# Kernel tuning notes

Hardware: AMD Instinct MI355X
Metric: run time of the kernel (lower is better)

The kernel has to match this reference:

```python
import jax, jax.numpy as jnp
import numpy as np

N_NODES = 100000
N_EDGES = 1_600_000
F_IN = 128
N_HEADS = 4
F_OUT = 32


def setup_inputs() -> dict:
    key = jax.random.key(0)
    k1, k2, k3, k4, k5 = jax.random.split(key, 5)
    h_in = jax.random.normal(k1, (N_NODES, F_IN), dtype=jnp.float32)
    edge_index = jax.random.randint(k2, (2, N_EDGES), 0, N_NODES, dtype=jnp.int64)
    # Xavier-uniform-ish scales
    W = jax.random.normal(k3, (F_IN, N_HEADS * F_OUT), dtype=jnp.float32) * (1.0 / np.sqrt(F_IN))
    b = jnp.zeros((N_HEADS * F_OUT,), dtype=jnp.float32)
    a_src = jax.random.normal(k4, (N_HEADS, F_OUT), dtype=jnp.float32) * 0.1
    a_tgt = jax.random.normal(k5, (N_HEADS, F_OUT), dtype=jnp.float32) * 0.1
    return {"h_in": h_in, "edge_index": edge_index, "W": W, "b": b, "a_src": a_src, "a_tgt": a_tgt}


def reference(h_in, edge_index, W, b, a_src, a_tgt):
    # Eval mode: dropout is identity.
    src, tgt = edge_index[0], edge_index[1]
    # Shared linear projection: [N, H, F]
    h_proj = (h_in @ W + b).reshape(-1, N_HEADS, F_OUT)
    # Per-node attention score contributions: [N, H]
    score_src = jnp.einsum('nhf,hf->nh', h_proj, a_src)
    score_tgt = jnp.einsum('nhf,hf->nh', h_proj, a_tgt)
    # Edge-level scores (gather), LeakyReLU(0.2) as in the original: [E, H]
    e = jax.nn.leaky_relu(score_tgt[tgt] + score_src[src], negative_slope=0.2)
    # Segment softmax over incoming edges of each target node.
    # (Original uses raw exp without max subtraction; replicate faithfully.)
    exp_e = jnp.exp(e)
    denom = jax.ops.segment_sum(exp_e, tgt, num_segments=N_NODES)  # [N, H]
    alpha = exp_e / (denom[tgt] + 1e-16)                            # [E, H]
    # Weighted message aggregation: [N, H, F]
    msg = alpha[:, :, None] * h_proj[src]                           # [E, H, F]
    h_new = jax.ops.segment_sum(msg, tgt, num_segments=N_NODES)
    # concat=True branch: original computes activation(new_features) but returns
    # the UN-activated concatenated view (new_features_sigm is unused) -> replicate.
    return h_new.reshape(N_NODES, N_HEADS * F_OUT)
```

## Files before the change

kernel.cpp:

```cpp
#include <hip/hip_runtime.h>
#include <hip/hip_bf16.h>

typedef unsigned short u16;
typedef unsigned int u32;
typedef long long i64;
typedef __attribute__((ext_vector_type(8))) short s8v;
typedef __attribute__((ext_vector_type(4))) float f32x4;

#define SUBCAP 1023
#define BKT_CAP (8 * SUBCAP)

__device__ __forceinline__ float bf2f(u16 u) {
    union { u32 i; float f; } x; x.i = ((u32)u) << 16; return x.f;
}
__device__ __forceinline__ u16 f2bf(float f) {
    union { float f; u32 i; } x; x.f = f;
    u32 v = x.i;
    u32 r = v + 0x7FFFu + ((v >> 16) & 1u);
    return (u16)(r >> 16);
}
__device__ __forceinline__ int get_i(const void* p, size_t i, int m64) {
    return m64 ? (int)((const i64*)p)[i] : ((const int*)p)[i];
}
__device__ __forceinline__ float lrelu_clamp(float v) {
    v = v > 0.f ? v : 0.2f * v;
    return fminf(v, 80.f);
}

__global__ __launch_bounds__(256) void k_init(
    const u16* __restrict__ hin, const int* __restrict__ eidx, int* __restrict__ flags,
    const u16* __restrict__ W, const float* __restrict__ Wf,
    const float* __restrict__ biasf, const float* __restrict__ asrcf,
    const float* __restrict__ atgtf,
    u16* __restrict__ Wt, u16* __restrict__ Wt_hi, u16* __restrict__ Wt_lo,
    float* __restrict__ wa, float* __restrict__ ba,
    int* __restrict__ bucket_cnt, int ncnt)
{
    const int b = blockIdx.x, t = threadIdx.x;
    if (b == 0) {
        __shared__ int c1, c2;
        if (t == 0) { c1 = 0; c2 = 0; }
        __syncthreads();
        int l1 = 0, l2 = 0;
        for (int i = t; i < 8192; i += 256) {
            float v = bf2f(hin[i]);
            if (!(fabsf(v) <= 100.f)) l1++;
            if ((i & 1) && eidx[i] == 0) l2++;
        }
        atomicAdd(&c1, l1); atomicAdd(&c2, l2);
        __syncthreads();
        if (t == 0) {
            flags[0] = (c1 > 40) ? 1 : 0;
            flags[1] = (c2 > 3000) ? 1 : 0;
        }
    } else if (b <= 64) {
        int i = (b - 1) * 256 + t;
        int k = i >> 7, n = i & 127;
        Wt[(size_t)n * 128 + k] = W[(size_t)k * 128 + n];
        float wf = Wf[(size_t)k * 128 + n];
        u16 hi = f2bf(wf);
        Wt_hi[(size_t)n * 128 + k] = hi;
        Wt_lo[(size_t)n * 128 + k] = f2bf(wf - bf2f(hi));
    } else if (b <= 68) {
        int idx = (b - 65) * 256 + t;
        int sel = idx >> 9, rem = idx & 511;
        int h = rem >> 7, k = rem & 127;
        const float* av = sel ? atgtf : asrcf;
        float s = 0.f;
        #pragma unroll 8
        for (int f = 0; f < 32; f++)
            s += Wf[(size_t)k * 128 + h * 32 + f] * av[h * 32 + f];
        wa[idx] = s;
    } else {
        if (t < 8) {
            int sel = t >> 2, h = t & 3;
            const float* av = sel ? atgtf : asrcf;
            float s = 0.f;
            #pragma unroll 8
            for (int f = 0; f < 32; f++)
                s += biasf[h * 32 + f] * av[h * 32 + f];
            ba[t] = s;
        }
    }
    for (int i = b * 256 + t; i < ncnt; i += gridDim.x * 256) bucket_cnt[i] = 0;
}

__global__ __launch_bounds__(256) void k_bktA(
    const void* __restrict__ eidx, const int* __restrict__ flags,
    int* __restrict__ bucket_cnt, u32* __restrict__ bkt,
    int n_edges, int n_nodes, int nbk)
{
    __shared__ int2 ed[4096];
    __shared__ int lcnt[512];
    __shared__ int lpos[512];
    const int t = threadIdx.x;
    const int e0 = blockIdx.x * 4096;
    const int rep = blockIdx.x & 7;
    const int m64 = flags[1];
    const int nloc = min(4096, n_edges - e0);

    for (int i = t; i < 512; i += 256) lcnt[i] = 0;
    __syncthreads();

    for (int r = 0; r < 16; r++) {
        int i = r * 256 + t;
        if (i < nloc) {
            int e = e0 + i;
            int s  = get_i(eidx, e, m64);
            int tg = get_i(eidx, (size_t)n_edges + e, m64);
            s  = min(max(s, 0), n_nodes - 1);
            tg = min(max(tg, 0), n_nodes - 1);
            ed[i] = make_int2(s, tg);
            atomicAdd(&lcnt[tg >> 8], 1);
        }
    }
    __syncthreads();

    for (int bb = t; bb < nbk; bb += 256) {
        int c = lcnt[bb];
        lpos[bb] = c ? atomicAdd(&bucket_cnt[rep * 512 + bb], c) : 0;
    }
    __syncthreads();

    for (int r = 0; r < 16; r++) {
        int i = r * 256 + t;
        if (i < nloc) {
            int2 st = ed[i];
            int bb = st.y >> 8;
            int p = atomicAdd(&lpos[bb], 1);
            p = min(p, SUBCAP - 1);
            bkt[(size_t)bb * BKT_CAP + rep * SUBCAP + p] =
                ((u32)st.x << 8) | (u32)(st.y & 255);
        }
    }
}

__global__ __launch_bounds__(256) void k_bsort(
    const int* __restrict__ bucket_cnt, const u32* __restrict__ bkt,
    int* __restrict__ offs, int* __restrict__ src_sorted,
    int n_edges, int n_nodes, int nbk)
{
    __shared__ int s_a[512], s_b[512];
    __shared__ int tcnt[256], tpos[256];
    __shared__ int subcnt[8];
    __shared__ int Gb_sh, total_sh;
    const int t = threadIdx.x;
    const int b = blockIdx.x;

    for (int i = t; i < 512; i += 256) {
        int tot = 0;
        if (i < nbk) {
            #pragma unroll
            for (int r = 0; r < 8; r++) tot += min(bucket_cnt[r * 512 + i], SUBCAP);
        }
        s_a[i] = tot;
    }
    if (t < 8) subcnt[t] = min(bucket_cnt[t * 512 + b], SUBCAP);
    __syncthreads();

    int* pa = s_a; int* pb = s_b;
    for (int off = 1; off < 512; off <<= 1) {
        #pragma unroll
        for (int k = 0; k < 2; k++) {
            int i = t + k * 256;
            pb[i] = pa[i] + (i >= off ? pa[i - off] : 0);
        }
        __syncthreads();
        int* sw = pa; pa = pb; pb = sw;
    }
    if (t == 0) {
        int run = 0;
        #pragma unroll
        for (int r = 0; r < 8; r++) run += subcnt[r];
        Gb_sh = pa[b] - run;
        total_sh = pa[511];
    }
    __syncthreads();
    const int Gb = Gb_sh, total = total_sh;

    tcnt[t] = 0;
    __syncthreads();
    const u32* mybkt = bkt + (size_t)b * BKT_CAP;
    #pragma unroll
    for (int r = 0; r < 8; r++) {
        const int c = subcnt[r];
        const u32* sub = mybkt + r * SUBCAP;
        for (int i = t; i < c; i += 256)
            atomicAdd(&tcnt[sub[i] & 255], 1);
    }
    __syncthreads();

    int own = tcnt[t];
    s_a[t] = own;
    __syncthreads();
    for (int off = 1; off < 256; off <<= 1) {
        int x = (t >= off) ? s_a[t - off] : 0;
        __syncthreads();
        s_a[t] += x;
        __syncthreads();
    }
    const int texcl = s_a[t] - own;

    const int tgt_id = b * 256 + t;
    if (tgt_id < n_nodes) offs[tgt_id] = Gb + texcl;
    if (b == 0 && t == 0) offs[n_nodes] = total;
    tpos[t] = Gb + texcl;
    __syncthreads();
    #pragma unroll
    for (int r = 0; r < 8; r++) {
        const int c = subcnt[r];
        const u32* sub = mybkt + r * SUBCAP;
        for (int i = t; i < c; i += 256) {
            u32 v = sub[i];
            int p = atomicAdd(&tpos[v & 255], 1);
            src_sorted[p] = (int)(v >> 8);
        }
    }
}

__global__ __launch_bounds__(256) void k_proj_mfma(
    const u16* __restrict__ hin, const u16* __restrict__ Wt,
    const u16* __restrict__ bias, const u16* __restrict__ a_src,
    const u16* __restrict__ a_tgt, const int* __restrict__ flags,
    u16* __restrict__ hp, float* __restrict__ ssrc, float* __restrict__ stgt,
    int M)
{
    if (flags[0]) return;
    const int lane = threadIdx.x & 63;
    const int q = lane >> 4, col = lane & 15;
    const int row0 = blockIdx.x * 64 + (threadIdx.x >> 6) * 16;
    if (row0 >= M) return;

    const int arow = min(row0 + col, M - 1);
    f32x4 acc[8];
    #pragma unroll
    for (int ct = 0; ct < 8; ct++) acc[ct] = (f32x4){0.f, 0.f, 0.f, 0.f};

    #pragma unroll
    for (int kc = 0; kc < 4; kc++) {
        s8v afrag = *(const s8v*)(hin + (size_t)arow * 128 + kc * 32 + q * 8);
        #pragma unroll
        for (int ct = 0; ct < 8; ct++) {
            s8v bfrag = *(const s8v*)(Wt + (size_t)(ct * 16 + col) * 128 + kc * 32 + q * 8);
            acc[ct] = __builtin_amdgcn_mfma_f32_16x16x32_bf16(afrag, bfrag, acc[ct], 0, 0, 0);
        }
    }

    float bb[8], as[8], at[8];
    #pragma unroll
    for (int ct = 0; ct < 8; ct++) {
        int c = ct * 16 + col;
        bb[ct] = bf2f(bias[c]);
        as[ct] = bf2f(a_src[c]);
        at[ct] = bf2f(a_tgt[c]);
    }

    #pragma unroll
    for (int r = 0; r < 4; r++) {
        int row = row0 + q * 4 + r;
        float ps0 = 0.f, ps1 = 0.f, ps2 = 0.f, ps3 = 0.f;
        float pt0 = 0.f, pt1 = 0.f, pt2 = 0.f, pt3 = 0.f;
        float ov[8];
        #pragma unroll
        for (int ct = 0; ct < 8; ct++) {
            float v = acc[ct][r] + bb[ct];
            ov[ct] = v;
            float s = v * as[ct], t2 = v * at[ct];
            if (ct < 2)      { ps0 += s; pt0 += t2; }
            else if (ct < 4) { ps1 += s; pt1 += t2; }
            else if (ct < 6) { ps2 += s; pt2 += t2; }
            else             { ps3 += s; pt3 += t2; }
        }
        if (row < M) {
            union { ushort4 h[2]; uint4 qv; } pk;
            pk.h[0] = make_ushort4(f2bf(ov[0]), f2bf(ov[1]), f2bf(ov[2]), f2bf(ov[3]));
            pk.h[1] = make_ushort4(f2bf(ov[4]), f2bf(ov[5]), f2bf(ov[6]), f2bf(ov[7]));
            *(uint4*)(hp + (size_t)row * 128 + col * 8) = pk.qv;
        }
        #pragma unroll
        for (int m = 1; m < 16; m <<= 1) {
            ps0 += __shfl_xor(ps0, m); ps1 += __shfl_xor(ps1, m);
            ps2 += __shfl_xor(ps2, m); ps3 += __shfl_xor(ps3, m);
            pt0 += __shfl_xor(pt0, m); pt1 += __shfl_xor(pt1, m);
            pt2 += __shfl_xor(pt2, m); pt3 += __shfl_xor(pt3, m);
        }
        if (row < M && col < 4) {
            float vs = col == 0 ? ps0 : col == 1 ? ps1 : col == 2 ? ps2 : ps3;
            float vt = col == 0 ? pt0 : col == 1 ? pt1 : col == 2 ? pt2 : pt3;
            ssrc[(size_t)row * 4 + col] = vs;
            stgt[(size_t)row * 4 + col] = vt;
        }
    }
}

__global__ __launch_bounds__(256) void k_proj_fm(
    const float* __restrict__ hin, const u16* __restrict__ Wt_hi,
    const u16* __restrict__ Wt_lo, const float* __restrict__ biasf,
    const float* __restrict__ wa, const float* __restrict__ ba,
    const int* __restrict__ flags,
    u16* __restrict__ hp, float* __restrict__ ssrc, float* __restrict__ stgt,
    int M)
{
    if (!flags[0]) return;
    __shared__ float wal[1032];
    const int t = threadIdx.x;
    for (int i = t; i < 1024; i += 256) wal[i] = wa[i];
    if (t < 8) wal[1024 + t] = ba[t];
    __syncthreads();

    const int lane = t & 63;
    const int q = lane >> 4, col = lane & 15;
    const int row0 = blockIdx.x * 64 + (t >> 6) * 16;
    if (row0 >= M) return;
    const int arow = min(row0 + col, M - 1);

    f32x4 acc[8];
    #pragma unroll
    for (int ct = 0; ct < 8; ct++) acc[ct] = (f32x4){0.f, 0.f, 0.f, 0.f};
    float ps[4] = {0.f, 0.f, 0.f, 0.f}, pt[4] = {0.f, 0.f, 0.f, 0.f};

    #pragma unroll
    for (int kc = 0; kc < 4; kc++) {
        const int ko = kc * 32 + q * 8;
        const float* hrow = hin + (size_t)arow * 128 + ko;
        float4 hva = *(const float4*)hrow;
        float4 hvb = *(const float4*)(hrow + 4);
        float hv[8] = {hva.x, hva.y, hva.z, hva.w, hvb.x, hvb.y, hvb.z, hvb.w};
        s8v ahi, alo;
        #pragma unroll
        for (int j = 0; j < 8; j++) {
            u16 hi = f2bf(hv[j]);
            ahi[j] = (short)hi;
            alo[j] = (short)f2bf(hv[j] - bf2f(hi));
        }
        #pragma unroll
        for (int ct = 0; ct < 8; ct++) {
            const size_t boff = (size_t)(ct * 16 + col) * 128 + ko;
            s8v bhi = *(const s8v*)(Wt_hi + boff);
            s8v blo = *(const s8v*)(Wt_lo + boff);
            acc[ct] = __builtin_amdgcn_mfma_f32_16x16x32_bf16(ahi, bhi, acc[ct], 0, 0, 0);
            acc[ct] = __builtin_amdgcn_mfma_f32_16x16x32_bf16(ahi, blo, acc[ct], 0, 0, 0);
            acc[ct] = __builtin_amdgcn_mfma_f32_16x16x32_bf16(alo, bhi, acc[ct], 0, 0, 0);
        }
        #pragma unroll
        for (int h = 0; h < 4; h++) {
            float4 sa = *(const float4*)&wal[h * 128 + ko];
            float4 sb = *(const float4*)&wal[h * 128 + ko + 4];
            ps[h] += hv[0] * sa.x + hv[1] * sa.y + hv[2] * sa.z + hv[3] * sa.w
                   + hv[4] * sb.x + hv[5] * sb.y + hv[6] * sb.z + hv[7] * sb.w;
            float4 ta = *(const float4*)&wal[512 + h * 128 + ko];
            float4 tb = *(const float4*)&wal[512 + h * 128 + ko + 4];
            pt[h] += hv[0] * ta.x + hv[1] * ta.y + hv[2] * ta.z + hv[3] * ta.w
                   + hv[4] * tb.x + hv[5] * tb.y + hv[6] * tb.z + hv[7] * tb.w;
        }
    }

    #pragma unroll
    for (int h = 0; h < 4; h++) {
        ps[h] += __shfl_xor(ps[h], 16); ps[h] += __shfl_xor(ps[h], 32);
        pt[h] += __shfl_xor(pt[h], 16); pt[h] += __shfl_xor(pt[h], 32);
    }
    if (q == 0 && row0 + col < M) {
        #pragma unroll
        for (int h = 0; h < 4; h++) {
            ssrc[(size_t)(row0 + col) * 4 + h] = ps[h] + wal[1024 + h];
            stgt[(size_t)(row0 + col) * 4 + h] = pt[h] + wal[1028 + h];
        }
    }

    float bb[8];
    #pragma unroll
    for (int ct = 0; ct < 8; ct++) bb[ct] = biasf[ct * 16 + col];
    #pragma unroll
    for (int r = 0; r < 4; r++) {
        int row = row0 + q * 4 + r;
        if (row < M) {
            union { ushort4 h[2]; uint4 qv; } pk;
            pk.h[0] = make_ushort4(f2bf(acc[0][r] + bb[0]), f2bf(acc[1][r] + bb[1]),
                                   f2bf(acc[2][r] + bb[2]), f2bf(acc[3][r] + bb[3]));
            pk.h[1] = make_ushort4(f2bf(acc[4][r] + bb[4]), f2bf(acc[5][r] + bb[5]),
                                   f2bf(acc[6][r] + bb[6]), f2bf(acc[7][r] + bb[7]));
            *(uint4*)(hp + (size_t)row * 128 + col * 8) = pk.qv;
        }
    }
}

__global__ __launch_bounds__(256) void k_agg_csr(
    const int* __restrict__ offs, const int* __restrict__ src_sorted,
    const float* __restrict__ ssrc, const float* __restrict__ stgt,
    const void* __restrict__ hp, void* __restrict__ out,
    const int* __restrict__ flags, int n_nodes)
{
    __shared__ u16 ob[4][128];
    __shared__ float obf[4][128];
    const int wave = threadIdx.x >> 6;
    int wid = (blockIdx.x * 256 + threadIdx.x) >> 6;
    wid = min(wid, n_nodes - 1);
    const int lane = threadIdx.x & 63;
    const int fp32 = flags[0];
    const int d0 = offs[wid], d1 = offs[wid + 1];

    const int sub = lane >> 4;
    const int li = lane & 15;
    const u16* hpb = (const u16*)hp;
    const float4* ssrc4 = (const float4*)ssrc;
    const float4 st4 = ((const float4*)stgt)[wid];
    const int deg = d1 - d0;

    float a[8] = {};
    auto accum = [&](float4 w, uint4 v) {
        a[0] += w.x * bf2f((u16)(v.x & 0xffff));
        a[1] += w.x * bf2f((u16)(v.x >> 16));
        a[2] += w.y * bf2f((u16)(v.y & 0xffff));
        a[3] += w.y * bf2f((u16)(v.y >> 16));
        a[4] += w.z * bf2f((u16)(v.z & 0xffff));
        a[5] += w.z * bf2f((u16)(v.z >> 16));
        a[6] += w.w * bf2f((u16)(v.w & 0xffff));
        a[7] += w.w * bf2f((u16)(v.w >> 16));
    };

    const int nh = min(deg, 64);
    int my_s = 0;
    float4 my_w = make_float4(0.f, 0.f, 0.f, 0.f);
    if (nh > 0) {
        my_s = src_sorted[d0 + min(lane, nh - 1)];
        float4 cs = ssrc4[my_s];
        if (lane < nh) {
            my_w = make_float4(__expf(lrelu_clamp(cs.x + st4.x)),
                               __expf(lrelu_clamp(cs.y + st4.y)),
                               __expf(lrelu_clamp(cs.z + st4.z)),
                               __expf(lrelu_clamp(cs.w + st4.w)));
        }
    }

    const int ns = (nh + 3) >> 2;
    auto sload = [&](int k, uint4& vv) {
        if (k < ns) {
            int s = __shfl(my_s, k * 4 + sub);
            vv = *(const uint4*)(hpb + (size_t)s * 128 + li * 8);
        }
    };
    auto sacc = [&](int k, uint4 vv) {
        if (k < ns) {
            int idx = k * 4 + sub;
            float4 w;
            w.x = __shfl(my_w.x, idx);
            w.y = __shfl(my_w.y, idx);
            w.z = __shfl(my_w.z, idx);
            w.w = __shfl(my_w.w, idx);
            accum(w, vv);
        }
    };
    uint4 v0{}, v1{}, v2{}, v3{}, v4{}, v5{}, v6{}, v7{};
    sload(0, v0); sload(1, v1); sload(2, v2); sload(3, v3);
    sload(4, v4); sload(5, v5); sload(6, v6); sload(7, v7);
    sacc(0, v0); sload(8, v0);
    sacc(1, v1); sload(9, v1);
    sacc(2, v2); sload(10, v2);
    sacc(3, v3); sload(11, v3);
    sacc(4, v4); sload(12, v4);
    sacc(5, v5); sload(13, v5);
    sacc(6, v6); sload(14, v6);
    sacc(7, v7); sload(15, v7);
    sacc(8, v0); sacc(9, v1); sacc(10, v2); sacc(11, v3);
    sacc(12, v4); sacc(13, v5); sacc(14, v6); sacc(15, v7);

    float4 es_t = make_float4(0.f, 0.f, 0.f, 0.f);
    if (deg > 64) {
        for (int e = d0 + 64; e < d1; e += 4) {
            int idx = e + sub;
            int ok = idx < d1;
            int s = src_sorted[ok ? idx : d1 - 1];
            uint4 v = *(const uint4*)(hpb + (size_t)s * 128 + li * 8);
            float4 cs = ssrc4[s];
            float4 w = make_float4(__expf(lrelu_clamp(cs.x + st4.x)),
                                   __expf(lrelu_clamp(cs.y + st4.y)),
                                   __expf(lrelu_clamp(cs.z + st4.z)),
                                   __expf(lrelu_clamp(cs.w + st4.w)));
            if (!ok) w = make_float4(0.f, 0.f, 0.f, 0.f);
            accum(w, v);
            es_t.x += w.x; es_t.y += w.y; es_t.z += w.z; es_t.w += w.w;
        }
    }

    float4 es = my_w;
    #pragma unroll
    for (int m = 1; m < 16; m <<= 1) {
        es.x += __shfl_xor(es.x, m);
        es.y += __shfl_xor(es.y, m);
        es.z += __shfl_xor(es.z, m);
        es.w += __shfl_xor(es.w, m);
    }
    es.x += es_t.x; es.y += es_t.y; es.z += es_t.z; es.w += es_t.w;

    #pragma unroll
    for (int m = 0; m < 8; m++) {
        a[m] += __shfl_xor(a[m], 16);
        a[m] += __shfl_xor(a[m], 32);
    }
    es.x += __shfl_xor(es.x, 16); es.x += __shfl_xor(es.x, 32);
    es.y += __shfl_xor(es.y, 16); es.y += __shfl_xor(es.y, 32);
    es.z += __shfl_xor(es.z, 16); es.z += __shfl_xor(es.z, 32);
    es.w += __shfl_xor(es.w, 16); es.w += __shfl_xor(es.w, 32);

    float inv4[4] = {1.f / (es.x + 1e-16f), 1.f / (es.y + 1e-16f),
                     1.f / (es.z + 1e-16f), 1.f / (es.w + 1e-16f)};

    if (!fp32) {
        if (sub == 0) {
            #pragma unroll
            for (int m = 0; m < 8; m++)
                ob[wave][m * 16 + li] = f2bf(a[m] * inv4[m >> 1]);
        }
        __syncthreads();
        if (sub == 0) {
            uint4 ov = *(const uint4*)&ob[wave][li * 8];
            *(uint4*)((u16*)out + (size_t)wid * 128 + li * 8) = ov;
        }
    } else {
        if (sub == 0) {
            #pragma unroll
            for (int m = 0; m < 8; m++)
                obf[wave][m * 16 + li] = a[m] * inv4[m >> 1];
        }
        __syncthreads();
        float* of = (float*)out + (size_t)wid * 128;
        *(float2*)(of + lane * 2) = make_float2(obf[wave][lane * 2],
                                                obf[wave][lane * 2 + 1]);
    }
}

extern "C" void kernel_launch(void* const* d_in, const int* in_sizes, int n_in,
                              void* d_out, int out_size, void* d_ws, size_t ws_size,
                              hipStream_t stream)
{
    const void* h_in  = d_in[0];
    const void* eidx  = d_in[1];
    const void* W     = d_in[2];
    const void* bias  = d_in[3];
    const void* a_src = d_in[4];
    const void* a_tgt = d_in[5];

    const int n_nodes = in_sizes[0] / 128;
    const int n_edges = in_sizes[1] / 2;
    const int nbk = (n_nodes + 255) >> 8;
    const int nba = (n_edges + 4095) / 4096;

    char* p = (char*)d_ws;
    auto alloc = [&](size_t bytes) { char* q = p; p += (bytes + 255) & ~(size_t)255; return q; };
    int*   flags      = (int*)  alloc(256);
    void*  hp         = (void*) alloc((size_t)n_nodes * 128 * sizeof(float));
    u16*   Wt         = (u16*)  alloc(128 * 128 * sizeof(u16));
    u16*   Wt_hi      = (u16*)  alloc(128 * 128 * sizeof(u16));
    u16*   Wt_lo      = (u16*)  alloc(128 * 128 * sizeof(u16));
    float* wa         = (float*)alloc(1024 * sizeof(float));
    float* ba         = (float*)alloc(8 * sizeof(float));
    float* ssrc       = (float*)alloc((size_t)n_nodes * 4 * sizeof(float));
    float* stgt       = (float*)alloc((size_t)n_nodes * 4 * sizeof(float));
    int*   offs       = (int*)  alloc(((size_t)n_nodes + 1) * sizeof(int));
    int*   bucket_cnt = (int*)  alloc(8 * 512 * sizeof(int));
    int*   src_sorted = (int*)  alloc((size_t)n_edges * sizeof(int));

    size_t bkt_bytes = (size_t)nbk * BKT_CAP * sizeof(u32);
    u32* bkt;
    if (bkt_bytes <= (size_t)n_nodes * 128 * 2)
        bkt = (u32*)((char*)hp + (size_t)n_nodes * 128 * 2);
    else
        bkt = (u32*)alloc(bkt_bytes);

    k_init     <<<70, 256, 0, stream>>>((const u16*)h_in, (const int*)eidx, flags,
                                        (const u16*)W, (const float*)W,
                                        (const float*)bias, (const float*)a_src,
                                        (const float*)a_tgt,
                                        Wt, Wt_hi, Wt_lo, wa, ba,
                                        bucket_cnt, 8 * 512);
    k_bktA     <<<nba, 256, 0, stream>>>(eidx, flags, bucket_cnt, bkt,
                                         n_edges, n_nodes, nbk);
    k_bsort    <<<nbk, 256, 0, stream>>>(bucket_cnt, bkt, offs, src_sorted,
                                         n_edges, n_nodes, nbk);
    k_proj_mfma<<<(n_nodes + 63) / 64, 256, 0, stream>>>((const u16*)h_in, Wt, (const u16*)bias,
                                                         (const u16*)a_src, (const u16*)a_tgt,
                                                         flags, (u16*)hp, ssrc, stgt, n_nodes);
    k_proj_fm  <<<(n_nodes + 63) / 64, 256, 0, stream>>>((const float*)h_in, Wt_hi, Wt_lo,
                                                         (const float*)bias, wa, ba,
                                                         flags, (u16*)hp, ssrc, stgt, n_nodes);
    k_agg_csr  <<<(n_nodes + 3) / 4, 256, 0, stream>>>(offs, src_sorted, ssrc, stgt,
                                                       hp, d_out, flags, n_nodes);
}
```

Baseline: 307.9 us.

## Quantize projected features to int8 with per-row scale and merge projection kernels

The projected node features are stored as int8 with a per-row absmax scale instead of bf16, which halves the bytes gathered per edge in the aggregation kernel. The per-row scale is folded into the attention weights. The two projection kernels (bf16 and fp32 paths) are merged into one launch that branches on the flag, and the edge-bucketing kernel now uses 2048 edges per block. The cost is lower numeric precision: 8-bit quantization of the features may exceed the accuracy tolerance.

```diff
diff --git a/kernel.cpp b/kernel.cpp
--- a/kernel.cpp
+++ b/kernel.cpp
@@ -90,19 +90,19 @@
     int* __restrict__ bucket_cnt, u32* __restrict__ bkt,
     int n_edges, int n_nodes, int nbk)
 {
-    __shared__ int2 ed[4096];
+    __shared__ int2 ed[2048];
     __shared__ int lcnt[512];
     __shared__ int lpos[512];
     const int t = threadIdx.x;
-    const int e0 = blockIdx.x * 4096;
+    const int e0 = blockIdx.x * 2048;
     const int rep = blockIdx.x & 7;
     const int m64 = flags[1];
-    const int nloc = min(4096, n_edges - e0);
+    const int nloc = min(2048, n_edges - e0);
 
     for (int i = t; i < 512; i += 256) lcnt[i] = 0;
     __syncthreads();
 
-    for (int r = 0; r < 16; r++) {
+    for (int r = 0; r < 8; r++) {
         int i = r * 256 + t;
         if (i < nloc) {
             int e = e0 + i;
@@ -122,7 +122,7 @@
     }
     __syncthreads();
 
-    for (int r = 0; r < 16; r++) {
+    for (int r = 0; r < 8; r++) {
         int i = r * 256 + t;
         if (i < nloc) {
             int2 st = ed[i];
@@ -218,95 +218,24 @@
     }
 }
 
-__global__ __launch_bounds__(256) void k_proj_mfma(
-    const u16* __restrict__ hin, const u16* __restrict__ Wt,
-    const u16* __restrict__ bias, const u16* __restrict__ a_src,
-    const u16* __restrict__ a_tgt, const int* __restrict__ flags,
-    u16* __restrict__ hp, float* __restrict__ ssrc, float* __restrict__ stgt,
-    int M)
-{
-    if (flags[0]) return;
-    const int lane = threadIdx.x & 63;
-    const int q = lane >> 4, col = lane & 15;
-    const int row0 = blockIdx.x * 64 + (threadIdx.x >> 6) * 16;
-    if (row0 >= M) return;
-
-    const int arow = min(row0 + col, M - 1);
-    f32x4 acc[8];
-    #pragma unroll
-    for (int ct = 0; ct < 8; ct++) acc[ct] = (f32x4){0.f, 0.f, 0.f, 0.f};
-
-    #pragma unroll
-    for (int kc = 0; kc < 4; kc++) {
-        s8v afrag = *(const s8v*)(hin + (size_t)arow * 128 + kc * 32 + q * 8);
-        #pragma unroll
-        for (int ct = 0; ct < 8; ct++) {
-            s8v bfrag = *(const s8v*)(Wt + (size_t)(ct * 16 + col) * 128 + kc * 32 + q * 8);
-            acc[ct] = __builtin_amdgcn_mfma_f32_16x16x32_bf16(afrag, bfrag, acc[ct], 0, 0, 0);
-        }
-    }
-
-    float bb[8], as[8], at[8];
-    #pragma unroll
-    for (int ct = 0; ct < 8; ct++) {
-        int c = ct * 16 + col;
-        bb[ct] = bf2f(bias[c]);
-        as[ct] = bf2f(a_src[c]);
-        at[ct] = bf2f(a_tgt[c]);
-    }
-
-    #pragma unroll
-    for (int r = 0; r < 4; r++) {
-        int row = row0 + q * 4 + r;
-        float ps0 = 0.f, ps1 = 0.f, ps2 = 0.f, ps3 = 0.f;
-        float pt0 = 0.f, pt1 = 0.f, pt2 = 0.f, pt3 = 0.f;
-        float ov[8];
-        #pragma unroll
-        for (int ct = 0; ct < 8; ct++) {
-            float v = acc[ct][r] + bb[ct];
-            ov[ct] = v;
-            float s = v * as[ct], t2 = v * at[ct];
-            if (ct < 2)      { ps0 += s; pt0 += t2; }
-            else if (ct < 4) { ps1 += s; pt1 += t2; }
-            else if (ct < 6) { ps2 += s; pt2 += t2; }
-            else             { ps3 += s; pt3 += t2; }
-        }
-        if (row < M) {
-            union { ushort4 h[2]; uint4 qv; } pk;
-            pk.h[0] = make_ushort4(f2bf(ov[0]), f2bf(ov[1]), f2bf(ov[2]), f2bf(ov[3]));
-            pk.h[1] = make_ushort4(f2bf(ov[4]), f2bf(ov[5]), f2bf(ov[6]), f2bf(ov[7]));
-            *(uint4*)(hp + (size_t)row * 128 + col * 8) = pk.qv;
-        }
-        #pragma unroll
-        for (int m = 1; m < 16; m <<= 1) {
-            ps0 += __shfl_xor(ps0, m); ps1 += __shfl_xor(ps1, m);
-            ps2 += __shfl_xor(ps2, m); ps3 += __shfl_xor(ps3, m);
-            pt0 += __shfl_xor(pt0, m); pt1 += __shfl_xor(pt1, m);
-            pt2 += __shfl_xor(pt2, m); pt3 += __shfl_xor(pt3, m);
-        }
-        if (row < M && col < 4) {
-            float vs = col == 0 ? ps0 : col == 1 ? ps1 : col == 2 ? ps2 : ps3;
-            float vt = col == 0 ? pt0 : col == 1 ? pt1 : col == 2 ? pt2 : pt3;
-            ssrc[(size_t)row * 4 + col] = vs;
-            stgt[(size_t)row * 4 + col] = vt;
-        }
-    }
-}
-
-__global__ __launch_bounds__(256) void k_proj_fm(
-    const float* __restrict__ hin, const u16* __restrict__ Wt_hi,
-    const u16* __restrict__ Wt_lo, const float* __restrict__ biasf,
+__global__ __launch_bounds__(256) void k_proj(
+    const void* __restrict__ hin_v, const u16* __restrict__ Wt,
+    const u16* __restrict__ Wt_hi, const u16* __restrict__ Wt_lo,
+    const void* __restrict__ bias_v, const void* __restrict__ a_src_v,
+    const void* __restrict__ a_tgt_v,
     const float* __restrict__ wa, const float* __restrict__ ba,
     const int* __restrict__ flags,
-    u16* __restrict__ hp, float* __restrict__ ssrc, float* __restrict__ stgt,
-    int M)
+    signed char* __restrict__ hp8, float* __restrict__ sc,
+    float* __restrict__ ssrc, float* __restrict__ stgt, int M)
 {
-    if (!flags[0]) return;
     __shared__ float wal[1032];
     const int t = threadIdx.x;
-    for (int i = t; i < 1024; i += 256) wal[i] = wa[i];
-    if (t < 8) wal[1024 + t] = ba[t];
-    __syncthreads();
+    const int fp32 = flags[0];
+    if (fp32) {
+        for (int i = t; i < 1024; i += 256) wal[i] = wa[i];
+        if (t < 8) wal[1024 + t] = ba[t];
+        __syncthreads();
+    }
 
     const int lane = t & 63;
     const int q = lane >> 4, col = lane & 15;
@@ -317,70 +246,139 @@
     f32x4 acc[8];
     #pragma unroll
     for (int ct = 0; ct < 8; ct++) acc[ct] = (f32x4){0.f, 0.f, 0.f, 0.f};
-    float ps[4] = {0.f, 0.f, 0.f, 0.f}, pt[4] = {0.f, 0.f, 0.f, 0.f};
-
-    #pragma unroll
-    for (int kc = 0; kc < 4; kc++) {
-        const int ko = kc * 32 + q * 8;
-        const float* hrow = hin + (size_t)arow * 128 + ko;
-        float4 hva = *(const float4*)hrow;
-        float4 hvb = *(const float4*)(hrow + 4);
-        float hv[8] = {hva.x, hva.y, hva.z, hva.w, hvb.x, hvb.y, hvb.z, hvb.w};
-        s8v ahi, alo;
-        #pragma unroll
-        for (int j = 0; j < 8; j++) {
-            u16 hi = f2bf(hv[j]);
-            ahi[j] = (short)hi;
-            alo[j] = (short)f2bf(hv[j] - bf2f(hi));
-        }
+
+    auto store_row = [&](int row, const float ov[8]) {
+        float amax = 0.f;
+        #pragma unroll
+        for (int ct = 0; ct < 8; ct++) amax = fmaxf(amax, fabsf(ov[ct]));
+        #pragma unroll
+        for (int m = 1; m < 16; m <<= 1)
+            amax = fmaxf(amax, __shfl_xor(amax, m));
+        if (row < M) {
+            float inv = amax > 0.f ? 127.f / amax : 0.f;
+            union { signed char c[8]; uint2 u; } pk;
+            #pragma unroll
+            for (int ct = 0; ct < 8; ct++)
+                pk.c[ct] = (signed char)(int)rintf(ov[ct] * inv);
+            *(uint2*)(hp8 + (size_t)row * 128 + col * 8) = pk.u;
+            if (col == 0) sc[row] = amax * (1.f / 127.f);
+        }
+    };
+
+    if (!fp32) {
+        const u16* hin = (const u16*)hin_v;
+        const u16* bias = (const u16*)bias_v;
+        const u16* a_src = (const u16*)a_src_v;
+        const u16* a_tgt = (const u16*)a_tgt_v;
+        #pragma unroll
+        for (int kc = 0; kc < 4; kc++) {
+            s8v afrag = *(const s8v*)(hin + (size_t)arow * 128 + kc * 32 + q * 8);
+            #pragma unroll
+            for (int ct = 0; ct < 8; ct++) {
+                s8v bfrag = *(const s8v*)(Wt + (size_t)(ct * 16 + col) * 128 + kc * 32 + q * 8);
+                acc[ct] = __builtin_amdgcn_mfma_f32_16x16x32_bf16(afrag, bfrag, acc[ct], 0, 0, 0);
+            }
+        }
+        float bb[8], as[8], at[8];
         #pragma unroll
         for (int ct = 0; ct < 8; ct++) {
-            const size_t boff = (size_t)(ct * 16 + col) * 128 + ko;
-            s8v bhi = *(const s8v*)(Wt_hi + boff);
-            s8v blo = *(const s8v*)(Wt_lo + boff);
-            acc[ct] = __builtin_amdgcn_mfma_f32_16x16x32_bf16(ahi, bhi, acc[ct], 0, 0, 0);
-            acc[ct] = __builtin_amdgcn_mfma_f32_16x16x32_bf16(ahi, blo, acc[ct], 0, 0, 0);
-            acc[ct] = __builtin_amdgcn_mfma_f32_16x16x32_bf16(alo, bhi, acc[ct], 0, 0, 0);
+            int c = ct * 16 + col;
+            bb[ct] = bf2f(bias[c]);
+            as[ct] = bf2f(a_src[c]);
+            at[ct] = bf2f(a_tgt[c]);
+        }
+        #pragma unroll
+        for (int r = 0; r < 4; r++) {
+            int row = row0 + q * 4 + r;
+            float ps0 = 0.f, ps1 = 0.f, ps2 = 0.f, ps3 = 0.f;
+            float pt0 = 0.f, pt1 = 0.f, pt2 = 0.f, pt3 = 0.f;
+            float ov[8];
+            #pragma unroll
+            for (int ct = 0; ct < 8; ct++) {
+                float v = acc[ct][r] + bb[ct];
+                ov[ct] = v;
+                float s = v * as[ct], t2 = v * at[ct];
+                if (ct < 2)      { ps0 += s; pt0 += t2; }
+                else if (ct < 4) { ps1 += s; pt1 += t2; }
+                else if (ct < 6) { ps2 += s; pt2 += t2; }
+                else             { ps3 += s; pt3 += t2; }
+            }
+            store_row(row, ov);
+            #pragma unroll
+            for (int m = 1; m < 16; m <<= 1) {
+                ps0 += __shfl_xor(ps0, m); ps1 += __shfl_xor(ps1, m);
+                ps2 += __shfl_xor(ps2, m); ps3 += __shfl_xor(ps3, m);
+                pt0 += __shfl_xor(pt0, m); pt1 += __shfl_xor(pt1, m);
+                pt2 += __shfl_xor(pt2, m); pt3 += __shfl_xor(pt3, m);
+            }
+            if (row < M && col < 4) {
+                float vs = col == 0 ? ps0 : col == 1 ? ps1 : col == 2 ? ps2 : ps3;
+                float vt = col == 0 ? pt0 : col == 1 ? pt1 : col == 2 ? pt2 : pt3;
+                ssrc[(size_t)row * 4 + col] = vs;
+                stgt[(size_t)row * 4 + col] = vt;
+            }
+        }
+    } else {
+        const float* hin = (const float*)hin_v;
+        const float* biasf = (const float*)bias_v;
+        float ps[4] = {0.f, 0.f, 0.f, 0.f}, pt[4] = {0.f, 0.f, 0.f, 0.f};
+        #pragma unroll
+        for (int kc = 0; kc < 4; kc++) {
+            const int ko = kc * 32 + q * 8;
+            const float* hrow = hin + (size_t)arow * 128 + ko;
+            float4 hva = *(const float4*)hrow;
+            float4 hvb = *(const float4*)(hrow + 4);
+            float hv[8] = {hva.x, hva.y, hva.z, hva.w, hvb.x, hvb.y, hvb.z, hvb.w};
+            s8v ahi, alo;
+            #pragma unroll
+            for (int j = 0; j < 8; j++) {
+                u16 hi = f2bf(hv[j]);
+                ahi[j] = (short)hi;
+                alo[j] = (short)f2bf(hv[j] - bf2f(hi));
+            }
+            #pragma unroll
+            for (int ct = 0; ct < 8; ct++) {
+                const size_t boff = (size_t)(ct * 16 + col) * 128 + ko;
+                s8v bhi = *(const s8v*)(Wt_hi + boff);
+                s8v blo = *(const s8v*)(Wt_lo + boff);
+                acc[ct] = __builtin_amdgcn_mfma_f32_16x16x32_bf16(ahi, bhi, acc[ct], 0, 0, 0);
+                acc[ct] = __builtin_amdgcn_mfma_f32_16x16x32_bf16(ahi, blo, acc[ct], 0, 0, 0);
+                acc[ct] = __builtin_amdgcn_mfma_f32_16x16x32_bf16(alo, bhi, acc[ct], 0, 0, 0);
+            }
+            #pragma unroll
+            for (int h = 0; h < 4; h++) {
+                float4 sa = *(const float4*)&wal[h * 128 + ko];
+                float4 sb = *(const float4*)&wal[h * 128 + ko + 4];
+                ps[h] += hv[0] * sa.x + hv[1] * sa.y + hv[2] * sa.z + hv[3] * sa.w
+                       + hv[4] * sb.x + hv[5] * sb.y + hv[6] * sb.z + hv[7] * sb.w;
+                float4 ta = *(const float4*)&wal[512 + h * 128 + ko];
+                float4 tb = *(const float4*)&wal[512 + h * 128 + ko + 4];
+                pt[h] += hv[0] * ta.x + hv[1] * ta.y + hv[2] * ta.z + hv[3] * ta.w
+                       + hv[4] * tb.x + hv[5] * tb.y + hv[6] * tb.z + hv[7] * tb.w;
+            }
         }
         #pragma unroll
         for (int h = 0; h < 4; h++) {
-            float4 sa = *(const float4*)&wal[h * 128 + ko];
-            float4 sb = *(const float4*)&wal[h * 128 + ko + 4];
-            ps[h] += hv[0] * sa.x + hv[1] * sa.y + hv[2] * sa.z + hv[3] * sa.w
-                   + hv[4] * sb.x + hv[5] * sb.y + hv[6] * sb.z + hv[7] * sb.w;
-            float4 ta = *(const float4*)&wal[512 + h * 128 + ko];
-            float4 tb = *(const float4*)&wal[512 + h * 128 + ko + 4];
-            pt[h] += hv[0] * ta.x + hv[1] * ta.y + hv[2] * ta.z + hv[3] * ta.w
-                   + hv[4] * tb.x + hv[5] * tb.y + hv[6] * tb.z + hv[7] * tb.w;
-        }
-    }
-
-    #pragma unroll
-    for (int h = 0; h < 4; h++) {
-        ps[h] += __shfl_xor(ps[h], 16); ps[h] += __shfl_xor(ps[h], 32);
-        pt[h] += __shfl_xor(pt[h], 16); pt[h] += __shfl_xor(pt[h], 32);
-    }
-    if (q == 0 && row0 + col < M) {
-        #pragma unroll
-        for (int h = 0; h < 4; h++) {
-            ssrc[(size_t)(row0 + col) * 4 + h] = ps[h] + wal[1024 + h];
-            stgt[(size_t)(row0 + col) * 4 + h] = pt[h] + wal[1028 + h];
-        }
-    }
-
-    float bb[8];
-    #pragma unroll
-    for (int ct = 0; ct < 8; ct++) bb[ct] = biasf[ct * 16 + col];
-    #pragma unroll
-    for (int r = 0; r < 4; r++) {
-        int row = row0 + q * 4 + r;
-        if (row < M) {
-            union { ushort4 h[2]; uint4 qv; } pk;
-            pk.h[0] = make_ushort4(f2bf(acc[0][r] + bb[0]), f2bf(acc[1][r] + bb[1]),
-                                   f2bf(acc[2][r] + bb[2]), f2bf(acc[3][r] + bb[3]));
-            pk.h[1] = make_ushort4(f2bf(acc[4][r] + bb[4]), f2bf(acc[5][r] + bb[5]),
-                                   f2bf(acc[6][r] + bb[6]), f2bf(acc[7][r] + bb[7]));
-            *(uint4*)(hp + (size_t)row * 128 + col * 8) = pk.qv;
+            ps[h] += __shfl_xor(ps[h], 16); ps[h] += __shfl_xor(ps[h], 32);
+            pt[h] += __shfl_xor(pt[h], 16); pt[h] += __shfl_xor(pt[h], 32);
+        }
+        if (q == 0 && row0 + col < M) {
+            #pragma unroll
+            for (int h = 0; h < 4; h++) {
+                ssrc[(size_t)(row0 + col) * 4 + h] = ps[h] + wal[1024 + h];
+                stgt[(size_t)(row0 + col) * 4 + h] = pt[h] + wal[1028 + h];
+            }
+        }
+        float bb[8];
+        #pragma unroll
+        for (int ct = 0; ct < 8; ct++) bb[ct] = biasf[ct * 16 + col];
+        #pragma unroll
+        for (int r = 0; r < 4; r++) {
+            int row = row0 + q * 4 + r;
+            float ov[8];
+            #pragma unroll
+            for (int ct = 0; ct < 8; ct++) ov[ct] = acc[ct][r] + bb[ct];
+            store_row(row, ov);
         }
     }
 }
@@ -388,8 +386,8 @@
 __global__ __launch_bounds__(256) void k_agg_csr(
     const int* __restrict__ offs, const int* __restrict__ src_sorted,
     const float* __restrict__ ssrc, const float* __restrict__ stgt,
-    const void* __restrict__ hp, void* __restrict__ out,
-    const int* __restrict__ flags, int n_nodes)
+    const float* __restrict__ sc, const signed char* __restrict__ hp8,
+    void* __restrict__ out, const int* __restrict__ flags, int n_nodes)
 {
     __shared__ u16 ob[4][128];
     __shared__ float obf[4][128];
@@ -402,56 +400,59 @@
 
     const int sub = lane >> 4;
     const int li = lane & 15;
-    const u16* hpb = (const u16*)hp;
     const float4* ssrc4 = (const float4*)ssrc;
     const float4 st4 = ((const float4*)stgt)[wid];
     const int deg = d1 - d0;
 
     float a[8] = {};
-    auto accum = [&](float4 w, uint4 v) {
-        a[0] += w.x * bf2f((u16)(v.x & 0xffff));
-        a[1] += w.x * bf2f((u16)(v.x >> 16));
-        a[2] += w.y * bf2f((u16)(v.y & 0xffff));
-        a[3] += w.y * bf2f((u16)(v.y >> 16));
-        a[4] += w.z * bf2f((u16)(v.z & 0xffff));
-        a[5] += w.z * bf2f((u16)(v.z >> 16));
-        a[6] += w.w * bf2f((u16)(v.w & 0xffff));
-        a[7] += w.w * bf2f((u16)(v.w >> 16));
+    auto accum = [&](float4 w, uint2 u) {
+        a[0] += w.x * (float)(int)(signed char)(u.x);
+        a[1] += w.x * (float)(int)(signed char)(u.x >> 8);
+        a[2] += w.y * (float)(int)(signed char)(u.x >> 16);
+        a[3] += w.y * (float)(int)(signed char)(u.x >> 24);
+        a[4] += w.z * (float)(int)(signed char)(u.y);
+        a[5] += w.z * (float)(int)(signed char)(u.y >> 8);
+        a[6] += w.w * (float)(int)(signed char)(u.y >> 16);
+        a[7] += w.w * (float)(int)(signed char)(u.y >> 24);
     };
 
     const int nh = min(deg, 64);
     int my_s = 0;
     float4 my_w = make_float4(0.f, 0.f, 0.f, 0.f);
+    float4 my_v = make_float4(0.f, 0.f, 0.f, 0.f);
     if (nh > 0) {
         my_s = src_sorted[d0 + min(lane, nh - 1)];
         float4 cs = ssrc4[my_s];
+        float sca = sc[my_s];
         if (lane < nh) {
             my_w = make_float4(__expf(lrelu_clamp(cs.x + st4.x)),
                                __expf(lrelu_clamp(cs.y + st4.y)),
                                __expf(lrelu_clamp(cs.z + st4.z)),
                                __expf(lrelu_clamp(cs.w + st4.w)));
+            my_v = make_float4(my_w.x * sca, my_w.y * sca,
+                               my_w.z * sca, my_w.w * sca);
         }
     }
 
     const int ns = (nh + 3) >> 2;
-    auto sload = [&](int k, uint4& vv) {
+    auto sload = [&](int k, uint2& vv) {
         if (k < ns) {
             int s = __shfl(my_s, k * 4 + sub);
-            vv = *(const uint4*)(hpb + (size_t)s * 128 + li * 8);
+            vv = *(const uint2*)(hp8 + (size_t)s * 128 + li * 8);
         }
     };
-    auto sacc = [&](int k, uint4 vv) {
+    auto sacc = [&](int k, uint2 vv) {
         if (k < ns) {
             int idx = k * 4 + sub;
             float4 w;
-            w.x = __shfl(my_w.x, idx);
-            w.y = __shfl(my_w.y, idx);
-            w.z = __shfl(my_w.z, idx);
-            w.w = __shfl(my_w.w, idx);
+            w.x = __shfl(my_v.x, idx);
+            w.y = __shfl(my_v.y, idx);
+            w.z = __shfl(my_v.z, idx);
+            w.w = __shfl(my_v.w, idx);
             accum(w, vv);
         }
     };
-    uint4 v0{}, v1{}, v2{}, v3{}, v4{}, v5{}, v6{}, v7{};
+    uint2 v0{}, v1{}, v2{}, v3{}, v4{}, v5{}, v6{}, v7{};
     sload(0, v0); sload(1, v1); sload(2, v2); sload(3, v3);
     sload(4, v4); sload(5, v5); sload(6, v6); sload(7, v7);
     sacc(0, v0); sload(8, v0);
@@ -471,14 +472,15 @@
             int idx = e + sub;
             int ok = idx < d1;
             int s = src_sorted[ok ? idx : d1 - 1];
-            uint4 v = *(const uint4*)(hpb + (size_t)s * 128 + li * 8);
+            uint2 v = *(const uint2*)(hp8 + (size_t)s * 128 + li * 8);
             float4 cs = ssrc4[s];
+            float sca = sc[s];
             float4 w = make_float4(__expf(lrelu_clamp(cs.x + st4.x)),
                                    __expf(lrelu_clamp(cs.y + st4.y)),
                                    __expf(lrelu_clamp(cs.z + st4.z)),
                                    __expf(lrelu_clamp(cs.w + st4.w)));
             if (!ok) w = make_float4(0.f, 0.f, 0.f, 0.f);
-            accum(w, v);
+            accum(make_float4(w.x * sca, w.y * sca, w.z * sca, w.w * sca), v);
             es_t.x += w.x; es_t.y += w.y; es_t.z += w.z; es_t.w += w.w;
         }
     }
@@ -544,7 +546,7 @@
     const int n_nodes = in_sizes[0] / 128;
     const int n_edges = in_sizes[1] / 2;
     const int nbk = (n_nodes + 255) >> 8;
-    const int nba = (n_edges + 4095) / 4096;
+    const int nba = (n_edges + 2047) / 2048;
 
     char* p = (char*)d_ws;
     auto alloc = [&](size_t bytes) { char* q = p; p += (bytes + 255) & ~(size_t)255; return q; };
@@ -555,6 +557,7 @@
     u16*   Wt_lo      = (u16*)  alloc(128 * 128 * sizeof(u16));
     float* wa         = (float*)alloc(1024 * sizeof(float));
     float* ba         = (float*)alloc(8 * sizeof(float));
+    float* sc         = (float*)alloc((size_t)n_nodes * sizeof(float));
     float* ssrc       = (float*)alloc((size_t)n_nodes * 4 * sizeof(float));
     float* stgt       = (float*)alloc((size_t)n_nodes * 4 * sizeof(float));
     int*   offs       = (int*)  alloc(((size_t)n_nodes + 1) * sizeof(int));
@@ -578,12 +581,11 @@
                                          n_edges, n_nodes, nbk);
     k_bsort    <<<nbk, 256, 0, stream>>>(bucket_cnt, bkt, offs, src_sorted,
                                          n_edges, n_nodes, nbk);
-    k_proj_mfma<<<(n_nodes + 63) / 64, 256, 0, stream>>>((const u16*)h_in, Wt, (const u16*)bias,
-                                                         (const u16*)a_src, (const u16*)a_tgt,
-                                                         flags, (u16*)hp, ssrc, stgt, n_nodes);
-    k_proj_fm  <<<(n_nodes + 63) / 64, 256, 0, stream>>>((const float*)h_in, Wt_hi, Wt_lo,
-                                                         (const float*)bias, wa, ba,
-                                                         flags, (u16*)hp, ssrc, stgt, n_nodes);
+    k_proj     <<<(n_nodes + 63) / 64, 256, 0, stream>>>(h_in, Wt, Wt_hi, Wt_lo,
+                                                         bias, a_src, a_tgt, wa, ba,
+                                                         flags, (signed char*)hp, sc,
+                                                         ssrc, stgt, n_nodes);
     k_agg_csr  <<<(n_nodes + 3) / 4, 256, 0, stream>>>(offs, src_sorted, ssrc, stgt,
-                                                       hp, d_out, flags, n_nodes);
-}
+                                                       sc, (const signed char*)hp,
+                                                       d_out, flags, n_nodes);
+}
```

Result: faster. 300.1 us (-2.5%).
